# Kernel tuning notes

Hardware: AMD Instinct MI355X
Metric: run time of the kernel (lower is better)

Reference implementation:

```python
import jax, jax.numpy as jnp
import numpy as np

N_USERS = 30000
N_ENT = 70000
N = N_USERS + N_ENT          # total graph nodes
E = 1_600_000                # edges (avg degree 16)
D = 64                       # embed_dim
B = 4096                     # scored user-item pairs
LEAKY_SLOPE = 0.01           # torch nn.LeakyReLU default
EPS = 1e-12                  # torch F.normalize default eps


def setup_inputs() -> dict:
    key = jax.random.key(0)
    ks = jax.random.split(key, 16)
    inp = {
        "edge_row": jax.random.randint(ks[0], (E,), 0, N, dtype=jnp.int32),
        "edge_col": jax.random.randint(ks[1], (E,), 0, N, dtype=jnp.int32),
        "edge_vals": jax.random.uniform(ks[2], (E,), dtype=jnp.float32) / 16.0,
        "user_embed": jax.random.normal(ks[3], (N_USERS, D), jnp.float32) * 0.1,
        "entity_embed": jax.random.normal(ks[4], (N_ENT, D), jnp.float32) * 0.1,
        "W1_0": jax.random.normal(ks[5], (D, 64), jnp.float32) * (1.0 / np.sqrt(D)),
        "b1_0": jnp.zeros((64,), jnp.float32),
        "W2_0": jax.random.normal(ks[6], (D, 64), jnp.float32) * (1.0 / np.sqrt(D)),
        "b2_0": jnp.zeros((64,), jnp.float32),
        "W1_1": jax.random.normal(ks[7], (64, 32), jnp.float32) * (1.0 / 8.0),
        "b1_1": jnp.zeros((32,), jnp.float32),
        "W2_1": jax.random.normal(ks[8], (64, 32), jnp.float32) * (1.0 / 8.0),
        "b2_1": jnp.zeros((32,), jnp.float32),
        "user_ids": jax.random.randint(ks[9], (B,), 0, N_USERS, dtype=jnp.int32),
        "item_ids": jax.random.randint(ks[10], (B,), 0, N_ENT, dtype=jnp.int32),
    }
    return inp


def _gnn_layer(feats, edge_row, edge_col, edge_vals, W1, b1, W2, b2):
    # sparse adj @ feats  ==  scatter-add of weighted source features to rows
    gathered = feats[edge_col] * edge_vals[:, None]          # (E, d_in)
    h_neigh = jax.ops.segment_sum(gathered, edge_row, num_segments=N)  # (N, d_in)
    term1 = (feats + h_neigh) @ W1 + b1
    term2 = (feats * h_neigh) @ W2 + b2
    h = jax.nn.leaky_relu(term1 + term2, negative_slope=LEAKY_SLOPE)
    # F.normalize(h, p=2, dim=1)
    norm = jnp.linalg.norm(h, axis=1, keepdims=True)
    return h / jnp.maximum(norm, EPS)


def reference(edge_row, edge_col, edge_vals, user_embed, entity_embed,
              W1_0, b1_0, W2_0, b2_0, W1_1, b1_1, W2_1, b2_1,
              user_ids, item_ids):
    a0 = jnp.concatenate([user_embed, entity_embed], axis=0)     # (N, 64)
    a1 = _gnn_layer(a0, edge_row, edge_col, edge_vals, W1_0, b1_0, W2_0, b2_0)  # (N, 64)
    a2 = _gnn_layer(a1, edge_row, edge_col, edge_vals, W1_1, b1_1, W2_1, b2_1)  # (N, 32)
    final = jnp.concatenate([a0, a1, a2], axis=1)                # (N, 160)
    u = final[user_ids]                                          # (B, 160)
    i = final[N_USERS + item_ids]                                # (B, 160)
    return jnp.sum(u * i, axis=1)                                # (B,)
```

## Files before the change

### kernel.cpp

```cpp
#include <hip/hip_runtime.h>
#include <hip/hip_bf16.h>
#include <math.h>

#define LEAKY 0.01f
#define SCAN_BLOCK 256
#define SCAN_ITEMS 4
#define SCAN_TILE (SCAN_BLOCK * SCAN_ITEMS)

struct __align__(8) Bf4 { __hip_bfloat16 a, b, c, d; };

__global__ void zero_i32(int* __restrict__ p, int n) {
    int i = blockIdx.x * blockDim.x + threadIdx.x;
    if (i < n) p[i] = 0;
}

__global__ void count_edges(const int* __restrict__ row, int E,
                            int* __restrict__ deg, int* __restrict__ rank) {
    int i = blockIdx.x * blockDim.x + threadIdx.x;
    if (i < E) rank[i] = atomicAdd(&deg[row[i]], 1);
}

__global__ __launch_bounds__(SCAN_BLOCK) void scan_phase1(
    const int* __restrict__ deg, int* __restrict__ blocksum, int N) {
    __shared__ int red[SCAN_BLOCK];
    int b = blockIdx.x, t = threadIdx.x;
    int base = b * SCAN_TILE + t * SCAN_ITEMS;
    int s = 0;
#pragma unroll
    for (int j = 0; j < SCAN_ITEMS; j++) {
        int i = base + j;
        if (i < N) s += deg[i];
    }
    red[t] = s;
    __syncthreads();
    for (int off = SCAN_BLOCK / 2; off > 0; off >>= 1) {
        if (t < off) red[t] += red[t + off];
        __syncthreads();
    }
    if (t == 0) blocksum[b] = red[0];
}

__global__ __launch_bounds__(1024) void scan_phase2(
    const int* __restrict__ blocksum, int* __restrict__ blockoff,
    int* __restrict__ row_ptr, int G, int N) {
    __shared__ int sums[1024];
    int t = threadIdx.x;
    sums[t] = (t < G) ? blocksum[t] : 0;
    __syncthreads();
    for (int off = 1; off < 1024; off <<= 1) {
        int v = (t >= off) ? sums[t - off] : 0;
        __syncthreads();
        sums[t] += v;
        __syncthreads();
    }
    if (t < G) blockoff[t] = (t == 0) ? 0 : sums[t - 1];
    if (t == G - 1) row_ptr[N] = sums[t];
}

__global__ __launch_bounds__(SCAN_BLOCK) void scan_phase3(
    const int* __restrict__ deg, const int* __restrict__ blockoff,
    int* __restrict__ row_ptr, int N) {
    __shared__ int red[SCAN_BLOCK];
    int b = blockIdx.x, t = threadIdx.x;
    int base = b * SCAN_TILE + t * SCAN_ITEMS;
    int v[SCAN_ITEMS];
    int s = 0;
#pragma unroll
    for (int j = 0; j < SCAN_ITEMS; j++) {
        int i = base + j;
        v[j] = (i < N) ? deg[i] : 0;
        s += v[j];
    }
    red[t] = s;
    __syncthreads();
    for (int off = 1; off < SCAN_BLOCK; off <<= 1) {
        int x = (t >= off) ? red[t - off] : 0;
        __syncthreads();
        red[t] += x;
        __syncthreads();
    }
    int run = blockoff[b] + ((t == 0) ? 0 : red[t - 1]);
#pragma unroll
    for (int j = 0; j < SCAN_ITEMS; j++) {
        int i = base + j;
        if (i < N) { row_ptr[i] = run; run += v[j]; }
    }
}

__global__ void build_a0(const float4* __restrict__ ue, const float4* __restrict__ ee,
                         float4* __restrict__ a0, __hip_bfloat16* __restrict__ a0b,
                         int nu4, int ntot4) {
    int i = blockIdx.x * blockDim.x + threadIdx.x;
    if (i < ntot4) {
        float4 v = (i < nu4) ? ue[i] : ee[i - nu4];
        a0[i] = v;
        Bf4 q = {__float2bfloat16(v.x), __float2bfloat16(v.y),
                 __float2bfloat16(v.z), __float2bfloat16(v.w)};
        *(Bf4*)&a0b[(size_t)i * 4] = q;
    }
}

__global__ void fill_csr(const int* __restrict__ row, const int* __restrict__ col,
                         const float* __restrict__ val, const int* __restrict__ rank,
                         const int* __restrict__ row_ptr, int E,
                         int2* __restrict__ csr) {
    int i = blockIdx.x * blockDim.x + threadIdx.x;
    if (i < E) {
        int p = row_ptr[row[i]] + rank[i];
        csr[p] = make_int2(col[i], __float_as_int(val[i]));
    }
}

__device__ __forceinline__ void fma4(float o[4], float sv, const float4& wv) {
    o[0] = fmaf(sv, wv.x, o[0]);
    o[1] = fmaf(sv, wv.y, o[1]);
    o[2] = fmaf(sv, wv.z, o[2]);
    o[3] = fmaf(sv, wv.w, o[3]);
}

template<int DOUT>
__global__ __launch_bounds__(256, 4) void gnn_layer(
    const float* __restrict__ feats, const __hip_bfloat16* __restrict__ featsb,
    const int2* __restrict__ csr, const int* __restrict__ row_ptr,
    const float* __restrict__ W1, const float* __restrict__ b1,
    const float* __restrict__ W2, const float* __restrict__ b2,
    float* __restrict__ out, __hip_bfloat16* __restrict__ outb, int N) {
    __shared__ __align__(16) float S[32 * 132];
    int wv = threadIdx.x >> 6, lane = threadIdx.x & 63;
    int nb = blockIdx.x * 32 + wv * 8;

    for (int ni = 0; ni < 8; ni++) {
        int node = nb + ni;
        if (node >= N) break;
        float x = feats[(size_t)node * 64 + lane];
        int e0 = row_ptr[node];
        int degn = row_ptr[node + 1] - e0;
        float acc = 0.f;
        int done = 0;
        while (done < degn) {
            int take = min(64, degn - done);
            int2 m = make_int2(0, 0);
            if (lane < take) m = csr[e0 + done + lane];
            int nch = (take + 7) >> 3;
            for (int c2 = 0; c2 < nch; c2++) {
                int base = c2 * 8;
                float fv[8], vv[8];
#pragma unroll
                for (int u = 0; u < 8; u++) {
                    int col = __shfl(m.x, base + u, 64);
                    vv[u] = __int_as_float(__shfl(m.y, base + u, 64));
                    fv[u] = __bfloat162float(featsb[(size_t)col * 64 + lane]);
                }
#pragma unroll
                for (int u = 0; u < 8; u++) acc = fmaf(vv[u], fv[u], acc);
            }
            done += take;
        }
        float* sp = &S[(wv * 8 + ni) * 132];
        sp[lane]      = x + acc;
        sp[64 + lane] = x * acc;
    }
    __threadfence_block();

    if constexpr (DOUT == 64) {
        int strip = lane & 15, g = lane >> 4;
        int d0 = strip * 4;
        float4 b1v = *(const float4*)&b1[d0];
        float4 b2v = *(const float4*)&b2[d0];
        float oa[4] = {b1v.x + b2v.x, b1v.y + b2v.y, b1v.z + b2v.z, b1v.w + b2v.w};
        float ob[4] = {oa[0], oa[1], oa[2], oa[3]};
        const float* spa = &S[(wv * 8 + 2 * g) * 132];
        const float* spb = spa + 132;
#pragma unroll
        for (int half = 0; half < 2; half++) {
            const float* W  = half ? W2 : W1;
            const float* sa = spa + half * 64;
            const float* sb = spb + half * 64;
#pragma unroll 2
            for (int k = 0; k < 64; k += 4) {
                float4 va = *(const float4*)&sa[k];
                float4 vb = *(const float4*)&sb[k];
                float4 wr0 = *(const float4*)&W[(k + 0) * 64 + d0];
                float4 wr1 = *(const float4*)&W[(k + 1) * 64 + d0];
                float4 wr2 = *(const float4*)&W[(k + 2) * 64 + d0];
                float4 wr3 = *(const float4*)&W[(k + 3) * 64 + d0];
                fma4(oa, va.x, wr0); fma4(oa, va.y, wr1);
                fma4(oa, va.z, wr2); fma4(oa, va.w, wr3);
                fma4(ob, vb.x, wr0); fma4(ob, vb.y, wr1);
                fma4(ob, vb.z, wr2); fma4(ob, vb.w, wr3);
            }
        }
#pragma unroll
        for (int t = 0; t < 2; t++) {
            float* o = t ? ob : oa;
            float h0 = (o[0] > 0.f) ? o[0] : LEAKY * o[0];
            float h1 = (o[1] > 0.f) ? o[1] : LEAKY * o[1];
            float h2 = (o[2] > 0.f) ? o[2] : LEAKY * o[2];
            float h3 = (o[3] > 0.f) ? o[3] : LEAKY * o[3];
            float ss = h0 * h0 + h1 * h1 + h2 * h2 + h3 * h3;
            ss += __shfl_xor(ss, 1, 64);
            ss += __shfl_xor(ss, 2, 64);
            ss += __shfl_xor(ss, 4, 64);
            ss += __shfl_xor(ss, 8, 64);
            float sc = 1.0f / fmaxf(sqrtf(ss), 1e-12f);
            int node = nb + 2 * g + t;
            if (node < N) {
                float4 r = {h0 * sc, h1 * sc, h2 * sc, h3 * sc};
                *(float4*)&out[(size_t)node * 64 + d0] = r;
                Bf4 q = {__float2bfloat16(r.x), __float2bfloat16(r.y),
                         __float2bfloat16(r.z), __float2bfloat16(r.w)};
                *(Bf4*)&outb[(size_t)node * 64 + d0] = q;
            }
        }
    } else {
        int strip = lane & 7, nI = lane >> 3;
        int d0 = strip * 4;
        float4 b1v = *(const float4*)&b1[d0];
        float4 b2v = *(const float4*)&b2[d0];
        float o[4] = {b1v.x + b2v.x, b1v.y + b2v.y, b1v.z + b2v.z, b1v.w + b2v.w};
        const float* sp = &S[(wv * 8 + nI) * 132];
#pragma unroll
        for (int half = 0; half < 2; half++) {
            const float* W  = half ? W2 : W1;
            const float* sv = sp + half * 64;
#pragma unroll 2
            for (int k = 0; k < 64; k += 4) {
                float4 v   = *(const float4*)&sv[k];
                float4 wr0 = *(const float4*)&W[(k + 0) * 32 + d0];
                float4 wr1 = *(const float4*)&W[(k + 1) * 32 + d0];
                float4 wr2 = *(const float4*)&W[(k + 2) * 32 + d0];
                float4 wr3 = *(const float4*)&W[(k + 3) * 32 + d0];
                fma4(o, v.x, wr0); fma4(o, v.y, wr1);
                fma4(o, v.z, wr2); fma4(o, v.w, wr3);
            }
        }
        float h0 = (o[0] > 0.f) ? o[0] : LEAKY * o[0];
        float h1 = (o[1] > 0.f) ? o[1] : LEAKY * o[1];
        float h2 = (o[2] > 0.f) ? o[2] : LEAKY * o[2];
        float h3 = (o[3] > 0.f) ? o[3] : LEAKY * o[3];
        float ss = h0 * h0 + h1 * h1 + h2 * h2 + h3 * h3;
        ss += __shfl_xor(ss, 1, 64);
        ss += __shfl_xor(ss, 2, 64);
        ss += __shfl_xor(ss, 4, 64);
        float sc = 1.0f / fmaxf(sqrtf(ss), 1e-12f);
        int node = nb + nI;
        if (node < N) {
            float4 r = {h0 * sc, h1 * sc, h2 * sc, h3 * sc};
            *(float4*)&out[(size_t)node * 32 + d0] = r;
        }
    }
}

__global__ __launch_bounds__(256) void score_pairs(
    const float* __restrict__ a0, const float* __restrict__ a1,
    const float* __restrict__ a2,
    const int* __restrict__ uid, const int* __restrict__ iid,
    float* __restrict__ out, int B, int NU) {
    int wave = threadIdx.x >> 6, lane = threadIdx.x & 63;
    int p = blockIdx.x * 4 + wave;
    if (p >= B) return;
    int u = uid[p], it = iid[p];
    size_t un = (size_t)u, in = (size_t)(NU + it);
    float s = a0[un * 64 + lane] * a0[in * 64 + lane];
    s = fmaf(a1[un * 64 + lane], a1[in * 64 + lane], s);
    if (lane < 32) s = fmaf(a2[un * 32 + lane], a2[in * 32 + lane], s);
#pragma unroll
    for (int m = 32; m >= 1; m >>= 1) s += __shfl_xor(s, m, 64);
    if (lane == 0) out[p] = s;
}

extern "C" void kernel_launch(void* const* d_in, const int* in_sizes, int n_in,
                              void* d_out, int out_size, void* d_ws, size_t ws_size,
                              hipStream_t stream) {
    const int*   edge_row  = (const int*)d_in[0];
    const int*   edge_col  = (const int*)d_in[1];
    const float* edge_vals = (const float*)d_in[2];
    const float* ue        = (const float*)d_in[3];
    const float* ee        = (const float*)d_in[4];
    const float* W1_0 = (const float*)d_in[5];
    const float* b1_0 = (const float*)d_in[6];
    const float* W2_0 = (const float*)d_in[7];
    const float* b2_0 = (const float*)d_in[8];
    const float* W1_1 = (const float*)d_in[9];
    const float* b1_1 = (const float*)d_in[10];
    const float* W2_1 = (const float*)d_in[11];
    const float* b2_1 = (const float*)d_in[12];
    const int*   uid  = (const int*)d_in[13];
    const int*   iid  = (const int*)d_in[14];
    float* out = (float*)d_out;

    const int E  = in_sizes[0];
    const int NU = in_sizes[3] / 64;
    const int NE = in_sizes[4] / 64;
    const int N  = NU + NE;
    const int B  = in_sizes[13];
    const int G  = (N + SCAN_TILE - 1) / SCAN_TILE;

    char* ws = (char*)d_ws;
    size_t off = 0;
    auto alloc = [&](size_t bytes) -> char* {
        char* p = ws + off;
        off = (off + bytes + 255) & ~(size_t)255;
        return p;
    };
    int*   deg      = (int*)alloc((size_t)N * 4);
    int*   rank     = (int*)alloc((size_t)E * 4);
    int*   row_ptr  = (int*)alloc((size_t)(N + 1) * 4);
    int*   blocksum = (int*)alloc((size_t)1024 * 4);
    int*   blockoff = (int*)alloc((size_t)1024 * 4);
    int2*  csr      = (int2*)alloc((size_t)E * 8);
    float* a0       = (float*)alloc((size_t)N * 64 * 4);
    float* a1       = (float*)alloc((size_t)N * 64 * 4);
    float* a2       = (float*)alloc((size_t)N * 32 * 4);
    __hip_bfloat16* a0b = (__hip_bfloat16*)alloc((size_t)N * 64 * 2);
    __hip_bfloat16* a1b = (__hip_bfloat16*)alloc((size_t)N * 64 * 2);
    (void)ws_size; (void)n_in; (void)out_size; (void)NE;

    zero_i32<<<(N + 255) / 256, 256, 0, stream>>>(deg, N);
    count_edges<<<(E + 255) / 256, 256, 0, stream>>>(edge_row, E, deg, rank);
    scan_phase1<<<G, SCAN_BLOCK, 0, stream>>>(deg, blocksum, N);
    scan_phase2<<<1, 1024, 0, stream>>>(blocksum, blockoff, row_ptr, G, N);
    scan_phase3<<<G, SCAN_BLOCK, 0, stream>>>(deg, blockoff, row_ptr, N);
    fill_csr<<<(E + 255) / 256, 256, 0, stream>>>(edge_row, edge_col, edge_vals,
                                                  rank, row_ptr, E, csr);
    int ntot4 = N * 16, nu4 = NU * 16;
    build_a0<<<(ntot4 + 255) / 256, 256, 0, stream>>>((const float4*)ue, (const float4*)ee,
                                                      (float4*)a0, a0b, nu4, ntot4);
    gnn_layer<64><<<(N + 31) / 32, 256, 0, stream>>>(a0, a0b, csr, row_ptr,
                                                     W1_0, b1_0, W2_0, b2_0, a1, a1b, N);
    gnn_layer<32><<<(N + 31) / 32, 256, 0, stream>>>(a1, a1b, csr, row_ptr,
                                                     W1_1, b1_1, W2_1, b2_1, a2, nullptr, N);
    score_pairs<<<(B + 3) / 4, 256, 0, stream>>>(a0, a1, a2, uid, iid, out, B, NU);
}
```

Measured before the change: 398.1 us.

## Gather four neighbors per wave with 8-byte bf16 loads and merge scan phases

The neighbor aggregation now splits each wave into four 16-lane groups. Each group handles a different edge and loads 4 bf16 features per lane as one ushort4, and the partial sums are reduced across groups with xor shuffles. This cuts the number of gather instructions and raises bytes per load, at the cost of an extra cross-lane reduction and 4 accumulators per lane. Separately, the single-block scan_phase2 is folded into scan_phase3, so each block redundantly scans the block sums and one kernel launch is removed. The fold assumes G is at most 256.

```diff
diff --git a/kernel.cpp b/kernel.cpp
--- a/kernel.cpp
+++ b/kernel.cpp
@@ -8,6 +8,10 @@
 #define SCAN_TILE (SCAN_BLOCK * SCAN_ITEMS)
 
 struct __align__(8) Bf4 { __hip_bfloat16 a, b, c, d; };
+
+__device__ __forceinline__ float bfu(unsigned short u) {
+    return __uint_as_float((unsigned)u << 16);
+}
 
 __global__ void zero_i32(int* __restrict__ p, int n) {
     int i = blockIdx.x * blockDim.x + threadIdx.x;
@@ -40,28 +44,23 @@
     if (t == 0) blocksum[b] = red[0];
 }
 
-__global__ __launch_bounds__(1024) void scan_phase2(
-    const int* __restrict__ blocksum, int* __restrict__ blockoff,
+__global__ __launch_bounds__(SCAN_BLOCK) void scan_phase3(
+    const int* __restrict__ deg, const int* __restrict__ blocksum,
     int* __restrict__ row_ptr, int G, int N) {
-    __shared__ int sums[1024];
-    int t = threadIdx.x;
-    sums[t] = (t < G) ? blocksum[t] : 0;
-    __syncthreads();
-    for (int off = 1; off < 1024; off <<= 1) {
-        int v = (t >= off) ? sums[t - off] : 0;
-        __syncthreads();
-        sums[t] += v;
-        __syncthreads();
-    }
-    if (t < G) blockoff[t] = (t == 0) ? 0 : sums[t - 1];
-    if (t == G - 1) row_ptr[N] = sums[t];
-}
-
-__global__ __launch_bounds__(SCAN_BLOCK) void scan_phase3(
-    const int* __restrict__ deg, const int* __restrict__ blockoff,
-    int* __restrict__ row_ptr, int N) {
+    __shared__ int bs[SCAN_BLOCK];
     __shared__ int red[SCAN_BLOCK];
     int b = blockIdx.x, t = threadIdx.x;
+    bs[t] = (t < G) ? blocksum[t] : 0;
+    __syncthreads();
+    for (int off = 1; off < SCAN_BLOCK; off <<= 1) {
+        int v = (t >= off) ? bs[t - off] : 0;
+        __syncthreads();
+        bs[t] += v;
+        __syncthreads();
+    }
+    int boff = (b == 0) ? 0 : bs[b - 1];
+    if (b == 0 && t == 0) row_ptr[N] = bs[G - 1];
+
     int base = b * SCAN_TILE + t * SCAN_ITEMS;
     int v[SCAN_ITEMS];
     int s = 0;
@@ -79,7 +78,7 @@
         red[t] += x;
         __syncthreads();
     }
-    int run = blockoff[b] + ((t == 0) ? 0 : red[t - 1]);
+    int run = boff + ((t == 0) ? 0 : red[t - 1]);
 #pragma unroll
     for (int j = 0; j < SCAN_ITEMS; j++) {
         int i = base + j;
@@ -127,49 +126,75 @@
     float* __restrict__ out, __hip_bfloat16* __restrict__ outb, int N) {
     __shared__ __align__(16) float S[32 * 132];
     int wv = threadIdx.x >> 6, lane = threadIdx.x & 63;
+    int g = lane >> 4, j = lane & 15;
+    const ushort* fb = (const ushort*)featsb;
     int nb = blockIdx.x * 32 + wv * 8;
 
     for (int ni = 0; ni < 8; ni++) {
         int node = nb + ni;
         if (node >= N) break;
-        float x = feats[(size_t)node * 64 + lane];
         int e0 = row_ptr[node];
         int degn = row_ptr[node + 1] - e0;
-        float acc = 0.f;
+        float a0_ = 0.f, a1_ = 0.f, a2_ = 0.f, a3_ = 0.f;
         int done = 0;
         while (done < degn) {
             int take = min(64, degn - done);
             int2 m = make_int2(0, 0);
             if (lane < take) m = csr[e0 + done + lane];
-            int nch = (take + 7) >> 3;
-            for (int c2 = 0; c2 < nch; c2++) {
-                int base = c2 * 8;
-                float fv[8], vv[8];
-#pragma unroll
-                for (int u = 0; u < 8; u++) {
-                    int col = __shfl(m.x, base + u, 64);
-                    vv[u] = __int_as_float(__shfl(m.y, base + u, 64));
-                    fv[u] = __bfloat162float(featsb[(size_t)col * 64 + lane]);
-                }
-#pragma unroll
-                for (int u = 0; u < 8; u++) acc = fmaf(vv[u], fv[u], acc);
+            int nsub = (take + 3) >> 2;
+            int c = 0;
+            for (; c + 4 <= nsub; c += 4) {
+                int s0 = c * 4 + g;
+                int c0 = __shfl(m.x, s0, 64);      float v0 = __int_as_float(__shfl(m.y, s0, 64));
+                int c1 = __shfl(m.x, s0 + 4, 64);  float v1 = __int_as_float(__shfl(m.y, s0 + 4, 64));
+                int c2 = __shfl(m.x, s0 + 8, 64);  float v2 = __int_as_float(__shfl(m.y, s0 + 8, 64));
+                int c3 = __shfl(m.x, s0 + 12, 64); float v3 = __int_as_float(__shfl(m.y, s0 + 12, 64));
+                ushort4 q0 = *(const ushort4*)&fb[(size_t)c0 * 64 + j * 4];
+                ushort4 q1 = *(const ushort4*)&fb[(size_t)c1 * 64 + j * 4];
+                ushort4 q2 = *(const ushort4*)&fb[(size_t)c2 * 64 + j * 4];
+                ushort4 q3 = *(const ushort4*)&fb[(size_t)c3 * 64 + j * 4];
+                a0_ = fmaf(v0, bfu(q0.x), a0_); a1_ = fmaf(v0, bfu(q0.y), a1_);
+                a2_ = fmaf(v0, bfu(q0.z), a2_); a3_ = fmaf(v0, bfu(q0.w), a3_);
+                a0_ = fmaf(v1, bfu(q1.x), a0_); a1_ = fmaf(v1, bfu(q1.y), a1_);
+                a2_ = fmaf(v1, bfu(q1.z), a2_); a3_ = fmaf(v1, bfu(q1.w), a3_);
+                a0_ = fmaf(v2, bfu(q2.x), a0_); a1_ = fmaf(v2, bfu(q2.y), a1_);
+                a2_ = fmaf(v2, bfu(q2.z), a2_); a3_ = fmaf(v2, bfu(q2.w), a3_);
+                a0_ = fmaf(v3, bfu(q3.x), a0_); a1_ = fmaf(v3, bfu(q3.y), a1_);
+                a2_ = fmaf(v3, bfu(q3.z), a2_); a3_ = fmaf(v3, bfu(q3.w), a3_);
+            }
+            for (; c < nsub; c++) {
+                int s0 = c * 4 + g;
+                int c0 = __shfl(m.x, s0, 64);
+                float v0 = __int_as_float(__shfl(m.y, s0, 64));
+                ushort4 q0 = *(const ushort4*)&fb[(size_t)c0 * 64 + j * 4];
+                a0_ = fmaf(v0, bfu(q0.x), a0_); a1_ = fmaf(v0, bfu(q0.y), a1_);
+                a2_ = fmaf(v0, bfu(q0.z), a2_); a3_ = fmaf(v0, bfu(q0.w), a3_);
             }
             done += take;
         }
-        float* sp = &S[(wv * 8 + ni) * 132];
-        sp[lane]      = x + acc;
-        sp[64 + lane] = x * acc;
+        a0_ += __shfl_xor(a0_, 16, 64); a0_ += __shfl_xor(a0_, 32, 64);
+        a1_ += __shfl_xor(a1_, 16, 64); a1_ += __shfl_xor(a1_, 32, 64);
+        a2_ += __shfl_xor(a2_, 16, 64); a2_ += __shfl_xor(a2_, 32, 64);
+        a3_ += __shfl_xor(a3_, 16, 64); a3_ += __shfl_xor(a3_, 32, 64);
+        if (g == 0) {
+            float4 xv = *(const float4*)&feats[(size_t)node * 64 + j * 4];
+            float* sp = &S[(wv * 8 + ni) * 132];
+            float4 s1v = {xv.x + a0_, xv.y + a1_, xv.z + a2_, xv.w + a3_};
+            float4 s2v = {xv.x * a0_, xv.y * a1_, xv.z * a2_, xv.w * a3_};
+            *(float4*)&sp[j * 4]      = s1v;
+            *(float4*)&sp[64 + j * 4] = s2v;
+        }
     }
     __threadfence_block();
 
     if constexpr (DOUT == 64) {
-        int strip = lane & 15, g = lane >> 4;
+        int strip = lane & 15, gg = lane >> 4;
         int d0 = strip * 4;
         float4 b1v = *(const float4*)&b1[d0];
         float4 b2v = *(const float4*)&b2[d0];
         float oa[4] = {b1v.x + b2v.x, b1v.y + b2v.y, b1v.z + b2v.z, b1v.w + b2v.w};
         float ob[4] = {oa[0], oa[1], oa[2], oa[3]};
-        const float* spa = &S[(wv * 8 + 2 * g) * 132];
+        const float* spa = &S[(wv * 8 + 2 * gg) * 132];
         const float* spb = spa + 132;
 #pragma unroll
         for (int half = 0; half < 2; half++) {
@@ -203,7 +228,7 @@
             ss += __shfl_xor(ss, 4, 64);
             ss += __shfl_xor(ss, 8, 64);
             float sc = 1.0f / fmaxf(sqrtf(ss), 1e-12f);
-            int node = nb + 2 * g + t;
+            int node = nb + 2 * gg + t;
             if (node < N) {
                 float4 r = {h0 * sc, h1 * sc, h2 * sc, h3 * sc};
                 *(float4*)&out[(size_t)node * 64 + d0] = r;
@@ -307,7 +332,6 @@
     int*   rank     = (int*)alloc((size_t)E * 4);
     int*   row_ptr  = (int*)alloc((size_t)(N + 1) * 4);
     int*   blocksum = (int*)alloc((size_t)1024 * 4);
-    int*   blockoff = (int*)alloc((size_t)1024 * 4);
     int2*  csr      = (int2*)alloc((size_t)E * 8);
     float* a0       = (float*)alloc((size_t)N * 64 * 4);
     float* a1       = (float*)alloc((size_t)N * 64 * 4);
@@ -319,8 +343,7 @@
     zero_i32<<<(N + 255) / 256, 256, 0, stream>>>(deg, N);
     count_edges<<<(E + 255) / 256, 256, 0, stream>>>(edge_row, E, deg, rank);
     scan_phase1<<<G, SCAN_BLOCK, 0, stream>>>(deg, blocksum, N);
-    scan_phase2<<<1, 1024, 0, stream>>>(blocksum, blockoff, row_ptr, G, N);
-    scan_phase3<<<G, SCAN_BLOCK, 0, stream>>>(deg, blockoff, row_ptr, N);
+    scan_phase3<<<G, SCAN_BLOCK, 0, stream>>>(deg, blocksum, row_ptr, G, N);
     fill_csr<<<(E + 255) / 256, 256, 0, stream>>>(edge_row, edge_col, edge_vals,
                                                   rank, row_ptr, E, csr);
     int ntot4 = N * 16, nu4 = NU * 16;
```

After: 405.7 us. About the same (+1.9%).

## Interleave gathers across four nodes per wave and fold scan phase2 into phase3

Applied to the files above, without the earlier changes.

The aggregation loop now processes four destination nodes at once per wave, interleaving their CSR and bf16 feature gathers so more independent memory loads are in flight. Layer 0 drops to 4 nodes per wave with a smaller shared tile, doubling the grid, and launch bounds now ask for 8 blocks per CU. The separate single-block scan_phase2 launch is removed: every phase3 block redundantly scans the block sums itself. The cost is divergence when the four nodes' degrees differ, more register pressure, and the in-block block-sum scan only covers up to 256 blocks.

```diff
diff --git a/kernel.cpp b/kernel.cpp
--- a/kernel.cpp
+++ b/kernel.cpp
@@ -8,6 +8,10 @@
 #define SCAN_TILE (SCAN_BLOCK * SCAN_ITEMS)
 
 struct __align__(8) Bf4 { __hip_bfloat16 a, b, c, d; };
+
+__device__ __forceinline__ float bfu(unsigned short u) {
+    return __uint_as_float((unsigned)u << 16);
+}
 
 __global__ void zero_i32(int* __restrict__ p, int n) {
     int i = blockIdx.x * blockDim.x + threadIdx.x;
@@ -40,28 +44,23 @@
     if (t == 0) blocksum[b] = red[0];
 }
 
-__global__ __launch_bounds__(1024) void scan_phase2(
-    const int* __restrict__ blocksum, int* __restrict__ blockoff,
+__global__ __launch_bounds__(SCAN_BLOCK) void scan_phase3(
+    const int* __restrict__ deg, const int* __restrict__ blocksum,
     int* __restrict__ row_ptr, int G, int N) {
-    __shared__ int sums[1024];
-    int t = threadIdx.x;
-    sums[t] = (t < G) ? blocksum[t] : 0;
-    __syncthreads();
-    for (int off = 1; off < 1024; off <<= 1) {
-        int v = (t >= off) ? sums[t - off] : 0;
-        __syncthreads();
-        sums[t] += v;
-        __syncthreads();
-    }
-    if (t < G) blockoff[t] = (t == 0) ? 0 : sums[t - 1];
-    if (t == G - 1) row_ptr[N] = sums[t];
-}
-
-__global__ __launch_bounds__(SCAN_BLOCK) void scan_phase3(
-    const int* __restrict__ deg, const int* __restrict__ blockoff,
-    int* __restrict__ row_ptr, int N) {
+    __shared__ int bs[SCAN_BLOCK];
     __shared__ int red[SCAN_BLOCK];
     int b = blockIdx.x, t = threadIdx.x;
+    bs[t] = (t < G) ? blocksum[t] : 0;
+    __syncthreads();
+    for (int off = 1; off < SCAN_BLOCK; off <<= 1) {
+        int v = (t >= off) ? bs[t - off] : 0;
+        __syncthreads();
+        bs[t] += v;
+        __syncthreads();
+    }
+    int boff = (b == 0) ? 0 : bs[b - 1];
+    if (b == 0 && t == 0) row_ptr[N] = bs[G - 1];
+
     int base = b * SCAN_TILE + t * SCAN_ITEMS;
     int v[SCAN_ITEMS];
     int s = 0;
@@ -79,7 +78,7 @@
         red[t] += x;
         __syncthreads();
     }
-    int run = blockoff[b] + ((t == 0) ? 0 : red[t - 1]);
+    int run = boff + ((t == 0) ? 0 : red[t - 1]);
 #pragma unroll
     for (int j = 0; j < SCAN_ITEMS; j++) {
         int i = base + j;
@@ -119,46 +118,63 @@
 }
 
 template<int DOUT>
-__global__ __launch_bounds__(256, 4) void gnn_layer(
+__global__ __launch_bounds__(256, 8) void gnn_layer(
     const float* __restrict__ feats, const __hip_bfloat16* __restrict__ featsb,
     const int2* __restrict__ csr, const int* __restrict__ row_ptr,
     const float* __restrict__ W1, const float* __restrict__ b1,
     const float* __restrict__ W2, const float* __restrict__ b2,
     float* __restrict__ out, __hip_bfloat16* __restrict__ outb, int N) {
-    __shared__ __align__(16) float S[32 * 132];
+    constexpr int NPW = (DOUT == 64) ? 4 : 8;
+    constexpr int NPB = NPW * 4;
+    __shared__ __align__(16) float S[NPB * 132];
     int wv = threadIdx.x >> 6, lane = threadIdx.x & 63;
-    int nb = blockIdx.x * 32 + wv * 8;
-
-    for (int ni = 0; ni < 8; ni++) {
-        int node = nb + ni;
-        if (node >= N) break;
-        float x = feats[(size_t)node * 64 + lane];
-        int e0 = row_ptr[node];
-        int degn = row_ptr[node + 1] - e0;
-        float acc = 0.f;
-        int done = 0;
-        while (done < degn) {
-            int take = min(64, degn - done);
-            int2 m = make_int2(0, 0);
-            if (lane < take) m = csr[e0 + done + lane];
-            int nch = (take + 7) >> 3;
-            for (int c2 = 0; c2 < nch; c2++) {
-                int base = c2 * 8;
-                float fv[8], vv[8];
-#pragma unroll
-                for (int u = 0; u < 8; u++) {
-                    int col = __shfl(m.x, base + u, 64);
-                    vv[u] = __int_as_float(__shfl(m.y, base + u, 64));
-                    fv[u] = __bfloat162float(featsb[(size_t)col * 64 + lane]);
+    const ushort* fb = (const ushort*)featsb;
+    int nb = blockIdx.x * NPB + wv * NPW;
+
+    for (int r = 0; r < NPW; r += 4) {
+        int n0 = nb + r;
+        int e0[4], dg[4];
+        float acc[4] = {0.f, 0.f, 0.f, 0.f};
+#pragma unroll
+        for (int i = 0; i < 4; i++) {
+            int node = n0 + i;
+            if (node < N) { e0[i] = row_ptr[node]; dg[i] = row_ptr[node + 1] - e0[i]; }
+            else          { e0[i] = 0; dg[i] = 0; }
+        }
+        int dmax = max(max(dg[0], dg[1]), max(dg[2], dg[3]));
+        for (int done = 0; done < dmax; done += 64) {
+            int2 m[4];
+#pragma unroll
+            for (int i = 0; i < 4; i++) {
+                int rem = dg[i] - done;
+                m[i] = (lane < rem) ? csr[e0[i] + done + lane] : make_int2(0, 0);
+            }
+            int cmax = min(dmax - done, 64);
+            for (int c = 0; c < cmax; c += 8) {
+#pragma unroll
+                for (int i = 0; i < 4; i++) {
+                    if (c < dg[i] - done) {
+                        float f[8], vv[8];
+#pragma unroll
+                        for (int u = 0; u < 8; u++) {
+                            int col = __shfl(m[i].x, c + u, 64);
+                            vv[u] = __int_as_float(__shfl(m[i].y, c + u, 64));
+                            f[u] = bfu(fb[(size_t)col * 64 + lane]);
+                        }
+#pragma unroll
+                        for (int u = 0; u < 8; u++) acc[i] = fmaf(vv[u], f[u], acc[i]);
+                    }
                 }
-#pragma unroll
-                for (int u = 0; u < 8; u++) acc = fmaf(vv[u], fv[u], acc);
             }
-            done += take;
-        }
-        float* sp = &S[(wv * 8 + ni) * 132];
-        sp[lane]      = x + acc;
-        sp[64 + lane] = x * acc;
+        }
+#pragma unroll
+        for (int i = 0; i < 4; i++) {
+            int node = n0 + i;
+            float x = (node < N) ? feats[(size_t)node * 64 + lane] : 0.f;
+            float* sp = &S[(wv * NPW + r + i) * 132];
+            sp[lane]      = x + acc[i];
+            sp[64 + lane] = x * acc[i];
+        }
     }
     __threadfence_block();
 
@@ -167,50 +183,40 @@
         int d0 = strip * 4;
         float4 b1v = *(const float4*)&b1[d0];
         float4 b2v = *(const float4*)&b2[d0];
-        float oa[4] = {b1v.x + b2v.x, b1v.y + b2v.y, b1v.z + b2v.z, b1v.w + b2v.w};
-        float ob[4] = {oa[0], oa[1], oa[2], oa[3]};
-        const float* spa = &S[(wv * 8 + 2 * g) * 132];
-        const float* spb = spa + 132;
+        float o[4] = {b1v.x + b2v.x, b1v.y + b2v.y, b1v.z + b2v.z, b1v.w + b2v.w};
+        const float* sp = &S[(wv * 4 + g) * 132];
 #pragma unroll
         for (int half = 0; half < 2; half++) {
             const float* W  = half ? W2 : W1;
-            const float* sa = spa + half * 64;
-            const float* sb = spb + half * 64;
+            const float* sv = sp + half * 64;
 #pragma unroll 2
             for (int k = 0; k < 64; k += 4) {
-                float4 va = *(const float4*)&sa[k];
-                float4 vb = *(const float4*)&sb[k];
+                float4 v   = *(const float4*)&sv[k];
                 float4 wr0 = *(const float4*)&W[(k + 0) * 64 + d0];
                 float4 wr1 = *(const float4*)&W[(k + 1) * 64 + d0];
                 float4 wr2 = *(const float4*)&W[(k + 2) * 64 + d0];
                 float4 wr3 = *(const float4*)&W[(k + 3) * 64 + d0];
-                fma4(oa, va.x, wr0); fma4(oa, va.y, wr1);
-                fma4(oa, va.z, wr2); fma4(oa, va.w, wr3);
-                fma4(ob, vb.x, wr0); fma4(ob, vb.y, wr1);
-                fma4(ob, vb.z, wr2); fma4(ob, vb.w, wr3);
+                fma4(o, v.x, wr0); fma4(o, v.y, wr1);
+                fma4(o, v.z, wr2); fma4(o, v.w, wr3);
             }
         }
-#pragma unroll
-        for (int t = 0; t < 2; t++) {
-            float* o = t ? ob : oa;
-            float h0 = (o[0] > 0.f) ? o[0] : LEAKY * o[0];
-            float h1 = (o[1] > 0.f) ? o[1] : LEAKY * o[1];
-            float h2 = (o[2] > 0.f) ? o[2] : LEAKY * o[2];
-            float h3 = (o[3] > 0.f) ? o[3] : LEAKY * o[3];
-            float ss = h0 * h0 + h1 * h1 + h2 * h2 + h3 * h3;
-            ss += __shfl_xor(ss, 1, 64);
-            ss += __shfl_xor(ss, 2, 64);
-            ss += __shfl_xor(ss, 4, 64);
-            ss += __shfl_xor(ss, 8, 64);
-            float sc = 1.0f / fmaxf(sqrtf(ss), 1e-12f);
-            int node = nb + 2 * g + t;
-            if (node < N) {
-                float4 r = {h0 * sc, h1 * sc, h2 * sc, h3 * sc};
-                *(float4*)&out[(size_t)node * 64 + d0] = r;
-                Bf4 q = {__float2bfloat16(r.x), __float2bfloat16(r.y),
-                         __float2bfloat16(r.z), __float2bfloat16(r.w)};
-                *(Bf4*)&outb[(size_t)node * 64 + d0] = q;
-            }
+        float h0 = (o[0] > 0.f) ? o[0] : LEAKY * o[0];
+        float h1 = (o[1] > 0.f) ? o[1] : LEAKY * o[1];
+        float h2 = (o[2] > 0.f) ? o[2] : LEAKY * o[2];
+        float h3 = (o[3] > 0.f) ? o[3] : LEAKY * o[3];
+        float ss = h0 * h0 + h1 * h1 + h2 * h2 + h3 * h3;
+        ss += __shfl_xor(ss, 1, 64);
+        ss += __shfl_xor(ss, 2, 64);
+        ss += __shfl_xor(ss, 4, 64);
+        ss += __shfl_xor(ss, 8, 64);
+        float sc = 1.0f / fmaxf(sqrtf(ss), 1e-12f);
+        int node = nb + g;
+        if (node < N) {
+            float4 rv = {h0 * sc, h1 * sc, h2 * sc, h3 * sc};
+            *(float4*)&out[(size_t)node * 64 + d0] = rv;
+            Bf4 q = {__float2bfloat16(rv.x), __float2bfloat16(rv.y),
+                     __float2bfloat16(rv.z), __float2bfloat16(rv.w)};
+            *(Bf4*)&outb[(size_t)node * 64 + d0] = q;
         }
     } else {
         int strip = lane & 7, nI = lane >> 3;
@@ -245,8 +251,8 @@
         float sc = 1.0f / fmaxf(sqrtf(ss), 1e-12f);
         int node = nb + nI;
         if (node < N) {
-            float4 r = {h0 * sc, h1 * sc, h2 * sc, h3 * sc};
-            *(float4*)&out[(size_t)node * 32 + d0] = r;
+            float4 rv = {h0 * sc, h1 * sc, h2 * sc, h3 * sc};
+            *(float4*)&out[(size_t)node * 32 + d0] = rv;
         }
     }
 }
@@ -307,7 +313,6 @@
     int*   rank     = (int*)alloc((size_t)E * 4);
     int*   row_ptr  = (int*)alloc((size_t)(N + 1) * 4);
     int*   blocksum = (int*)alloc((size_t)1024 * 4);
-    int*   blockoff = (int*)alloc((size_t)1024 * 4);
     int2*  csr      = (int2*)alloc((size_t)E * 8);
     float* a0       = (float*)alloc((size_t)N * 64 * 4);
     float* a1       = (float*)alloc((size_t)N * 64 * 4);
@@ -319,14 +324,13 @@
     zero_i32<<<(N + 255) / 256, 256, 0, stream>>>(deg, N);
     count_edges<<<(E + 255) / 256, 256, 0, stream>>>(edge_row, E, deg, rank);
     scan_phase1<<<G, SCAN_BLOCK, 0, stream>>>(deg, blocksum, N);
-    scan_phase2<<<1, 1024, 0, stream>>>(blocksum, blockoff, row_ptr, G, N);
-    scan_phase3<<<G, SCAN_BLOCK, 0, stream>>>(deg, blockoff, row_ptr, N);
+    scan_phase3<<<G, SCAN_BLOCK, 0, stream>>>(deg, blocksum, row_ptr, G, N);
     fill_csr<<<(E + 255) / 256, 256, 0, stream>>>(edge_row, edge_col, edge_vals,
                                                   rank, row_ptr, E, csr);
     int ntot4 = N * 16, nu4 = NU * 16;
     build_a0<<<(ntot4 + 255) / 256, 256, 0, stream>>>((const float4*)ue, (const float4*)ee,
                                                       (float4*)a0, a0b, nu4, ntot4);
-    gnn_layer<64><<<(N + 31) / 32, 256, 0, stream>>>(a0, a0b, csr, row_ptr,
+    gnn_layer<64><<<(N + 15) / 16, 256, 0, stream>>>(a0, a0b, csr, row_ptr,
                                                      W1_0, b1_0, W2_0, b2_0, a1, a1b, N);
     gnn_layer<32><<<(N + 31) / 32, 256, 0, stream>>>(a1, a1b, csr, row_ptr,
                                                      W1_1, b1_1, W2_1, b2_1, a2, nullptr, N);
```

After: 465.2 us. 1.17x slower.

## Fold scan phase2 into phase3, pre-shift CSR columns, restructure neighbor gather

Applied to the files above, without the earlier changes.

Removes the single-block scan_phase2 launch: each phase3 block now scans the block sums itself, which requires G<=256 (N=100000 gives G=98). CSR column indices are stored pre-multiplied by the bf16 row stride (col<<7) so the gather computes byte addresses directly. The aggregation loop now has every lane load 8 CSR entries per step as uniform loads instead of a coalesced load plus shuffles, then issues 8 independent bf16 feature loads, clamping the tail indices. Row pointers for a wave's 8 nodes are prefetched up front. The shifted column index overflows 32 bits for node counts above about 16M.

```diff
diff --git a/kernel.cpp b/kernel.cpp
--- a/kernel.cpp
+++ b/kernel.cpp
@@ -8,6 +8,10 @@
 #define SCAN_TILE (SCAN_BLOCK * SCAN_ITEMS)
 
 struct __align__(8) Bf4 { __hip_bfloat16 a, b, c, d; };
+
+__device__ __forceinline__ float bfu(unsigned short u) {
+    return __uint_as_float((unsigned)u << 16);
+}
 
 __global__ void zero_i32(int* __restrict__ p, int n) {
     int i = blockIdx.x * blockDim.x + threadIdx.x;
@@ -40,28 +44,23 @@
     if (t == 0) blocksum[b] = red[0];
 }
 
-__global__ __launch_bounds__(1024) void scan_phase2(
-    const int* __restrict__ blocksum, int* __restrict__ blockoff,
+__global__ __launch_bounds__(SCAN_BLOCK) void scan_phase3(
+    const int* __restrict__ deg, const int* __restrict__ blocksum,
     int* __restrict__ row_ptr, int G, int N) {
-    __shared__ int sums[1024];
-    int t = threadIdx.x;
-    sums[t] = (t < G) ? blocksum[t] : 0;
-    __syncthreads();
-    for (int off = 1; off < 1024; off <<= 1) {
-        int v = (t >= off) ? sums[t - off] : 0;
-        __syncthreads();
-        sums[t] += v;
-        __syncthreads();
-    }
-    if (t < G) blockoff[t] = (t == 0) ? 0 : sums[t - 1];
-    if (t == G - 1) row_ptr[N] = sums[t];
-}
-
-__global__ __launch_bounds__(SCAN_BLOCK) void scan_phase3(
-    const int* __restrict__ deg, const int* __restrict__ blockoff,
-    int* __restrict__ row_ptr, int N) {
+    __shared__ int bs[SCAN_BLOCK];
     __shared__ int red[SCAN_BLOCK];
     int b = blockIdx.x, t = threadIdx.x;
+    bs[t] = (t < G) ? blocksum[t] : 0;
+    __syncthreads();
+    for (int off = 1; off < SCAN_BLOCK; off <<= 1) {
+        int v = (t >= off) ? bs[t - off] : 0;
+        __syncthreads();
+        bs[t] += v;
+        __syncthreads();
+    }
+    int boff = (b == 0) ? 0 : bs[b - 1];
+    if (b == 0 && t == 0) row_ptr[N] = bs[G - 1];
+
     int base = b * SCAN_TILE + t * SCAN_ITEMS;
     int v[SCAN_ITEMS];
     int s = 0;
@@ -79,7 +78,7 @@
         red[t] += x;
         __syncthreads();
     }
-    int run = blockoff[b] + ((t == 0) ? 0 : red[t - 1]);
+    int run = boff + ((t == 0) ? 0 : red[t - 1]);
 #pragma unroll
     for (int j = 0; j < SCAN_ITEMS; j++) {
         int i = base + j;
@@ -107,7 +106,7 @@
     int i = blockIdx.x * blockDim.x + threadIdx.x;
     if (i < E) {
         int p = row_ptr[row[i]] + rank[i];
-        csr[p] = make_int2(col[i], __float_as_int(val[i]));
+        csr[p] = make_int2(col[i] << 7, __float_as_int(val[i]));
     }
 }
 
@@ -127,34 +126,40 @@
     float* __restrict__ out, __hip_bfloat16* __restrict__ outb, int N) {
     __shared__ __align__(16) float S[32 * 132];
     int wv = threadIdx.x >> 6, lane = threadIdx.x & 63;
+    const char* fbb = (const char*)featsb;
+    int l2 = lane << 1;
     int nb = blockIdx.x * 32 + wv * 8;
+
+    int rp[9];
+#pragma unroll
+    for (int i = 0; i <= 8; i++) {
+        int idx = nb + i;
+        rp[i] = row_ptr[(idx < N) ? idx : N];
+    }
 
     for (int ni = 0; ni < 8; ni++) {
         int node = nb + ni;
         if (node >= N) break;
         float x = feats[(size_t)node * 64 + lane];
-        int e0 = row_ptr[node];
-        int degn = row_ptr[node + 1] - e0;
+        int e0 = rp[ni], e1 = rp[ni + 1];
         float acc = 0.f;
-        int done = 0;
-        while (done < degn) {
-            int take = min(64, degn - done);
-            int2 m = make_int2(0, 0);
-            if (lane < take) m = csr[e0 + done + lane];
-            int nch = (take + 7) >> 3;
-            for (int c2 = 0; c2 < nch; c2++) {
-                int base = c2 * 8;
-                float fv[8], vv[8];
-#pragma unroll
-                for (int u = 0; u < 8; u++) {
-                    int col = __shfl(m.x, base + u, 64);
-                    vv[u] = __int_as_float(__shfl(m.y, base + u, 64));
-                    fv[u] = __bfloat162float(featsb[(size_t)col * 64 + lane]);
-                }
-#pragma unroll
-                for (int u = 0; u < 8; u++) acc = fmaf(vv[u], fv[u], acc);
-            }
-            done += take;
+        for (int e = e0; e < e1; e += 8) {
+            int last = e1 - 1;
+            int2 m[8];
+#pragma unroll
+            for (int u = 0; u < 8; u++) {
+                int ee = e + u;
+                m[u] = csr[(ee < last) ? ee : last];
+            }
+            float f[8];
+#pragma unroll
+            for (int u = 0; u < 8; u++)
+                f[u] = bfu(*(const ushort*)(fbb + (unsigned)m[u].x + l2));
+#pragma unroll
+            for (int u = 0; u < 8; u++) {
+                float v = (e + u < e1) ? __int_as_float(m[u].y) : 0.f;
+                acc = fmaf(v, f[u], acc);
+            }
         }
         float* sp = &S[(wv * 8 + ni) * 132];
         sp[lane]      = x + acc;
@@ -163,13 +168,13 @@
     __threadfence_block();
 
     if constexpr (DOUT == 64) {
-        int strip = lane & 15, g = lane >> 4;
+        int strip = lane & 15, gg = lane >> 4;
         int d0 = strip * 4;
         float4 b1v = *(const float4*)&b1[d0];
         float4 b2v = *(const float4*)&b2[d0];
         float oa[4] = {b1v.x + b2v.x, b1v.y + b2v.y, b1v.z + b2v.z, b1v.w + b2v.w};
         float ob[4] = {oa[0], oa[1], oa[2], oa[3]};
-        const float* spa = &S[(wv * 8 + 2 * g) * 132];
+        const float* spa = &S[(wv * 8 + 2 * gg) * 132];
         const float* spb = spa + 132;
 #pragma unroll
         for (int half = 0; half < 2; half++) {
@@ -203,12 +208,12 @@
             ss += __shfl_xor(ss, 4, 64);
             ss += __shfl_xor(ss, 8, 64);
             float sc = 1.0f / fmaxf(sqrtf(ss), 1e-12f);
-            int node = nb + 2 * g + t;
+            int node = nb + 2 * gg + t;
             if (node < N) {
-                float4 r = {h0 * sc, h1 * sc, h2 * sc, h3 * sc};
-                *(float4*)&out[(size_t)node * 64 + d0] = r;
-                Bf4 q = {__float2bfloat16(r.x), __float2bfloat16(r.y),
-                         __float2bfloat16(r.z), __float2bfloat16(r.w)};
+                float4 rv = {h0 * sc, h1 * sc, h2 * sc, h3 * sc};
+                *(float4*)&out[(size_t)node * 64 + d0] = rv;
+                Bf4 q = {__float2bfloat16(rv.x), __float2bfloat16(rv.y),
+                         __float2bfloat16(rv.z), __float2bfloat16(rv.w)};
                 *(Bf4*)&outb[(size_t)node * 64 + d0] = q;
             }
         }
@@ -245,8 +250,8 @@
         float sc = 1.0f / fmaxf(sqrtf(ss), 1e-12f);
         int node = nb + nI;
         if (node < N) {
-            float4 r = {h0 * sc, h1 * sc, h2 * sc, h3 * sc};
-            *(float4*)&out[(size_t)node * 32 + d0] = r;
+            float4 rv = {h0 * sc, h1 * sc, h2 * sc, h3 * sc};
+            *(float4*)&out[(size_t)node * 32 + d0] = rv;
         }
     }
 }
@@ -307,7 +312,6 @@
     int*   rank     = (int*)alloc((size_t)E * 4);
     int*   row_ptr  = (int*)alloc((size_t)(N + 1) * 4);
     int*   blocksum = (int*)alloc((size_t)1024 * 4);
-    int*   blockoff = (int*)alloc((size_t)1024 * 4);
     int2*  csr      = (int2*)alloc((size_t)E * 8);
     float* a0       = (float*)alloc((size_t)N * 64 * 4);
     float* a1       = (float*)alloc((size_t)N * 64 * 4);
@@ -319,8 +323,7 @@
     zero_i32<<<(N + 255) / 256, 256, 0, stream>>>(deg, N);
     count_edges<<<(E + 255) / 256, 256, 0, stream>>>(edge_row, E, deg, rank);
     scan_phase1<<<G, SCAN_BLOCK, 0, stream>>>(deg, blocksum, N);
-    scan_phase2<<<1, 1024, 0, stream>>>(blocksum, blockoff, row_ptr, G, N);
-    scan_phase3<<<G, SCAN_BLOCK, 0, stream>>>(deg, blockoff, row_ptr, N);
+    scan_phase3<<<G, SCAN_BLOCK, 0, stream>>>(deg, blocksum, row_ptr, G, N);
     fill_csr<<<(E + 255) / 256, 256, 0, stream>>>(edge_row, edge_col, edge_vals,
                                                   rank, row_ptr, E, csr);
     int ntot4 = N * 16, nu4 = NU * 16;
```

New measurement: 477.1 us. 19.9% more time.
